# Optimization experiments

Measured on AMD Instinct MI355X. Metric: run time of the kernel, lower is better.

Reference implementation:

```python
import jax, jax.numpy as jnp
import numpy as np

N_NODES = 100000
N_EDGES = 1600000
D = 128
BETA = 0.001
EPS = 1e-12  # F.normalize eps


def setup_inputs() -> dict:
    key = jax.random.key(0)
    k1, k2, k3, k4, k5, k6 = jax.random.split(key, 6)
    stdv = 1.0 / np.sqrt(D)
    return {
        "input": jax.random.normal(k1, (N_NODES, D), dtype=jnp.float32),
        "edge_rows": jax.random.randint(k2, (N_EDGES,), 0, N_NODES, dtype=jnp.int32),
        "edge_cols": jax.random.randint(k3, (N_EDGES,), 0, N_NODES, dtype=jnp.int32),
        "edge_vals": jax.random.uniform(k4, (N_EDGES,), dtype=jnp.float32),
        "weight": jax.random.uniform(k5, (D, D), minval=-stdv, maxval=stdv, dtype=jnp.float32),
        "bias": jax.random.uniform(k6, (D,), minval=-stdv, maxval=stdv, dtype=jnp.float32),
    }


def reference(input, edge_rows, edge_cols, edge_vals, weight, bias):
    # dense projection: [N, D]
    support = input @ weight
    # sparse neighbor aggregation: agg[i] = sum_{(i,j) in E} adj_val * support[j]
    msgs = edge_vals[:, None] * support[edge_cols]          # [E, D]
    agg = jax.ops.segment_sum(msgs, edge_rows, num_segments=input.shape[0])
    # beta-weighted residual blend
    out = BETA * input + (1.0 - BETA) * agg
    # row-wise L2 normalize (torch F.normalize, p=2, dim=1)
    norm = jnp.sqrt(jnp.sum(out * out, axis=1, keepdims=True))
    out = out / jnp.maximum(norm, EPS)
    # bias add
    return out + bias
```

## Files before the change

### kernel.cpp

```cpp
#include <hip/hip_runtime.h>

#define N_NODES 100000
#define N_EDGES 1600000
#define D 128
#define NB 1563
#define NSUB 8
#define SUBCAP 224
#define CAP (NSUB*SUBCAP)
#define NSLICE 8
#define SLICE_W 12500

typedef short bf16x8 __attribute__((ext_vector_type(8)));
typedef float f32x4 __attribute__((ext_vector_type(4)));

__device__ __forceinline__ unsigned short f2bf(float x){
  union { float f; unsigned u; } v; v.f = x;
  unsigned r = v.u + 0x7fffu + ((v.u >> 16) & 1u);
  return (unsigned short)(r >> 16);
}

__device__ __forceinline__ float bf2f(unsigned short h){
  union { unsigned u; float f; } v; v.u = ((unsigned)h) << 16;
  return v.f;
}

__global__ __launch_bounds__(256) void convert_input(const float4* __restrict__ in4,
                                                     ushort4* __restrict__ outb,
                                                     int* __restrict__ cursor,
                                                     const float* __restrict__ W,
                                                     unsigned short* __restrict__ WT){
  int i = blockIdx.x*256 + threadIdx.x;
  if (i < NSUB*NB) cursor[i] = 0;
  if (i < D*D){
    int k = i >> 7, c = i & 127;
    WT[c*128 + k] = f2bf(W[i]);
  }
  float4 a = in4[i];
  ushort4 h;
  h.x = f2bf(a.x); h.y = f2bf(a.y); h.z = f2bf(a.z); h.w = f2bf(a.w);
  outb[i] = h;
}

__global__ __launch_bounds__(256) void scatter_direct(const int* __restrict__ rows,
                                                      const int* __restrict__ cols,
                                                      const float* __restrict__ vals,
                                                      int* __restrict__ cursor,
                                                      int2* __restrict__ edges_s){
  int i = blockIdx.x*256 + threadIdx.x;
  int s = blockIdx.x & (NSUB-1);
  int r = rows[i];
  int b = r >> 6;
  int pos = atomicAdd(&cursor[s*NB + b], 1);
  if (pos < SUBCAP)
    edges_s[(size_t)b*CAP + s*SUBCAP + pos] =
        make_int2(cols[i] | ((r & 63) << 17), __float_as_int(vals[i]));
}

__global__ __launch_bounds__(512) void agg_final(const ushort4* __restrict__ inb4,
                                                 const int* __restrict__ cursor,
                                                 const int2* __restrict__ edges_g,
                                                 const unsigned short* __restrict__ WTg,
                                                 const float* __restrict__ bias,
                                                 float* __restrict__ out){
  __shared__ __align__(16) unsigned char pool[64*136*2];
  __shared__ unsigned short As[64*136];
  __shared__ int rs[NSLICE*64 + 1];
  __shared__ int cur[NSLICE*64];
  __shared__ int wsum[8];
  __shared__ float rsum[2][64];
  int2* st = (int2*)pool;
  unsigned short* Bs = (unsigned short*)pool;

  int t = threadIdx.x;
  int b = blockIdx.x;
  size_t base = (size_t)b * CAP;

  cur[t] = 0;
  __syncthreads();

  int2 held[NSUB];
  int hv = 0;
  #pragma unroll
  for (int s = 0; s < NSUB; ++s){
    int ms = cursor[s*NB + b];
    if (ms > SUBCAP) ms = SUBCAP;
    if (t < ms){
      int2 e = edges_g[base + s*SUBCAP + t];
      held[s] = e;
      hv |= (1 << s);
      int col = e.x & 0x1FFFF;
      int bin = (col / SLICE_W)*64 + (((unsigned)e.x) >> 17);
      atomicAdd(&cur[bin], 1);
    }
  }
  __syncthreads();

  {
    int c = cur[t];
    int w = t >> 6, lane = t & 63;
    int x = c;
    #pragma unroll
    for (int o = 1; o < 64; o <<= 1){
      int y = __shfl_up(x, o);
      if (lane >= o) x += y;
    }
    if (lane == 63) wsum[w] = x;
    __syncthreads();
    int pre = 0;
    #pragma unroll
    for (int ww = 0; ww < 8; ++ww)
      if (ww < w) pre += wsum[ww];
    int excl = pre + x - c;
    rs[t] = excl;
    cur[t] = excl;
    if (t == 511) rs[512] = excl + c;
  }
  __syncthreads();

  #pragma unroll
  for (int s = 0; s < NSUB; ++s){
    if (hv & (1 << s)){
      int2 e = held[s];
      int col = e.x & 0x1FFFF;
      int bin = (col / SLICE_W)*64 + (((unsigned)e.x) >> 17);
      int pos = atomicAdd(&cur[bin], 1);
      st[pos] = e;
    }
  }
  __syncthreads();

  int grp = t >> 5, l = t & 31;
  float4 r0 = make_float4(0.f,0.f,0.f,0.f);
  float4 r1 = make_float4(0.f,0.f,0.f,0.f);
  float4 r2 = make_float4(0.f,0.f,0.f,0.f);
  float4 r3 = make_float4(0.f,0.f,0.f,0.f);

#define EDGE_ACC(E) { \
    int col_ = (E).x & 0x1FFFF; \
    int j_ = (((unsigned)(E).x) >> 17) & 3; \
    float v_ = __int_as_float((E).y); \
    ushort4 X_ = inb4[(size_t)col_*32 + l]; \
    float f0_ = (j_==0)? v_ : 0.f; \
    float f1_ = (j_==1)? v_ : 0.f; \
    float f2_ = (j_==2)? v_ : 0.f; \
    float f3_ = (j_==3)? v_ : 0.f; \
    float xx_ = bf2f(X_.x), xy_ = bf2f(X_.y), xz_ = bf2f(X_.z), xw_ = bf2f(X_.w); \
    r0.x = fmaf(f0_, xx_, r0.x); r0.y = fmaf(f0_, xy_, r0.y); \
    r0.z = fmaf(f0_, xz_, r0.z); r0.w = fmaf(f0_, xw_, r0.w); \
    r1.x = fmaf(f1_, xx_, r1.x); r1.y = fmaf(f1_, xy_, r1.y); \
    r1.z = fmaf(f1_, xz_, r1.z); r1.w = fmaf(f1_, xw_, r1.w); \
    r2.x = fmaf(f2_, xx_, r2.x); r2.y = fmaf(f2_, xy_, r2.y); \
    r2.z = fmaf(f2_, xz_, r2.z); r2.w = fmaf(f2_, xw_, r2.w); \
    r3.x = fmaf(f3_, xx_, r3.x); r3.y = fmaf(f3_, xy_, r3.y); \
    r3.z = fmaf(f3_, xz_, r3.z); r3.w = fmaf(f3_, xw_, r3.w); }

  for (int s = 0; s < NSLICE; ++s){
    int bin0 = (s << 6) + (grp << 2);
    int e = rs[bin0];
    int end = rs[bin0 + 4];
    for (; e + 4 <= end; e += 4){
      int2 E0 = st[e+0], E1 = st[e+1], E2 = st[e+2], E3 = st[e+3];
      EDGE_ACC(E0); EDGE_ACC(E1); EDGE_ACC(E2); EDGE_ACC(E3);
    }
    for (; e < end; ++e){
      int2 E = st[e];
      EDGE_ACC(E);
    }
    __syncthreads();
  }
#undef EDGE_ACC

  {
    ushort4 h;
    h.x = f2bf(r0.x); h.y = f2bf(r0.y); h.z = f2bf(r0.z); h.w = f2bf(r0.w);
    *((ushort4*)&As[(grp*4+0)*136 + l*4]) = h;
    h.x = f2bf(r1.x); h.y = f2bf(r1.y); h.z = f2bf(r1.z); h.w = f2bf(r1.w);
    *((ushort4*)&As[(grp*4+1)*136 + l*4]) = h;
    h.x = f2bf(r2.x); h.y = f2bf(r2.y); h.z = f2bf(r2.z); h.w = f2bf(r2.w);
    *((ushort4*)&As[(grp*4+2)*136 + l*4]) = h;
    h.x = f2bf(r3.x); h.y = f2bf(r3.y); h.z = f2bf(r3.z); h.w = f2bf(r3.w);
    *((ushort4*)&As[(grp*4+3)*136 + l*4]) = h;
  }
  __syncthreads();

  int w = t >> 6, lane = t & 63;
  int wr = w >> 1, wc = w & 1;
  int q = lane >> 4, n = lane & 15;
  int block_row = b * 64;

  #pragma unroll
  for (int i = 0; i < 4; ++i){
    int idx4 = i*512 + t;
    int row = idx4 >> 5, k4 = idx4 & 31;
    int grow = block_row + row;
    ushort4 h = make_ushort4(0,0,0,0);
    if (grow < N_NODES) h = inb4[(size_t)grow*32 + k4];
    *((ushort4*)&Bs[row*136 + k4*4]) = h;
  }

  bf16x8 afr[4];
  #pragma unroll
  for (int ks = 0; ks < 4; ++ks)
    afr[ks] = *((const bf16x8*)&As[(wr*16 + n)*136 + ks*32 + q*8]);

  f32x4 acc[4];
  #pragma unroll
  for (int ct = 0; ct < 4; ++ct) acc[ct] = (f32x4){0.f, 0.f, 0.f, 0.f};
  #pragma unroll
  for (int ct = 0; ct < 4; ++ct){
    #pragma unroll
    for (int ks = 0; ks < 4; ++ks){
      bf16x8 bfr = *((const bf16x8*)(WTg + (wc*64 + ct*16 + n)*128 + ks*32 + q*8));
      acc[ct] = __builtin_amdgcn_mfma_f32_16x16x32_bf16(afr[ks], bfr, acc[ct], 0, 0, 0);
    }
  }
  __syncthreads();

  float v[4][4];
  float s[4] = {0.f, 0.f, 0.f, 0.f};
  #pragma unroll
  for (int reg = 0; reg < 4; ++reg){
    int row_local = wr*16 + q*4 + reg;
    #pragma unroll
    for (int ct = 0; ct < 4; ++ct){
      float inp = bf2f(Bs[row_local*136 + wc*64 + ct*16 + n]);
      float val = fmaf(0.999f, acc[ct][reg], 0.001f * inp);
      v[ct][reg] = val;
      s[reg] = fmaf(val, val, s[reg]);
    }
  }
  #pragma unroll
  for (int reg = 0; reg < 4; ++reg){
    float x = s[reg];
    x += __shfl_xor(x, 1);
    x += __shfl_xor(x, 2);
    x += __shfl_xor(x, 4);
    x += __shfl_xor(x, 8);
    s[reg] = x;
  }
  if (n == 0){
    #pragma unroll
    for (int reg = 0; reg < 4; ++reg)
      rsum[wc][wr*16 + q*4 + reg] = s[reg];
  }
  __syncthreads();

  #pragma unroll
  for (int reg = 0; reg < 4; ++reg){
    int row_local = wr*16 + q*4 + reg;
    int grow = block_row + row_local;
    if (grow >= N_NODES) continue;
    float tot = rsum[0][row_local] + rsum[1][row_local];
    float scale = 1.f / fmaxf(sqrtf(tot), 1e-12f);
    float* outrow = out + (size_t)grow * D;
    #pragma unroll
    for (int ct = 0; ct < 4; ++ct){
      int c = wc*64 + ct*16 + n;
      outrow[c] = fmaf(v[ct][reg], scale, bias[c]);
    }
  }
}

extern "C" void kernel_launch(void* const* d_in, const int* in_sizes, int n_in,
                              void* d_out, int out_size, void* d_ws, size_t ws_size,
                              hipStream_t stream){
  const float* input  = (const float*)d_in[0];
  const int*   erows  = (const int*)d_in[1];
  const int*   ecols  = (const int*)d_in[2];
  const float* evals  = (const float*)d_in[3];
  const float* weight = (const float*)d_in[4];
  const float* bias   = (const float*)d_in[5];
  float* out = (float*)d_out;

  int*   cursor    = (int*)d_ws;
  int2*  edges_s   = (int2*)(cursor + NSUB*NB);
  ushort4* inb     = (ushort4*)(edges_s + (size_t)NB*CAP);
  unsigned short* WTg = (unsigned short*)(inb + (size_t)N_NODES * 32);

  convert_input<<<12500, 256, 0, stream>>>((const float4*)input, inb, cursor, weight, WTg);
  scatter_direct<<<N_EDGES/256, 256, 0, stream>>>(erows, ecols, evals, cursor, edges_s);
  agg_final<<<NB, 512, 0, stream>>>((const ushort4*)inb, cursor, edges_s,
                                    WTg, bias, out);
}
```

Baseline: 308.4 us.

## Assign one 8-thread group per row instead of 32-thread group per four rows

The gather-accumulate phase now gives each destination row its own 8-lane group, with each lane loading four ushort4 chunks of the neighbor row. Before, a 32-lane group handled four rows and applied masked FMAs to all four accumulators for every edge. The change removes the 4x redundant FMA work from masking and stores plain column indices in the sorted edge list. The cost is more independent groups with their own edge-count imbalance, and less coalesced per-lane loads (8 lanes x 4 strided chunks instead of 32 contiguous lanes).

```diff
diff --git a/kernel.cpp b/kernel.cpp
--- a/kernel.cpp
+++ b/kernel.cpp
@@ -124,62 +124,59 @@
       int col = e.x & 0x1FFFF;
       int bin = (col / SLICE_W)*64 + (((unsigned)e.x) >> 17);
       int pos = atomicAdd(&cur[bin], 1);
-      st[pos] = e;
-    }
-  }
-  __syncthreads();
-
-  int grp = t >> 5, l = t & 31;
-  float4 r0 = make_float4(0.f,0.f,0.f,0.f);
-  float4 r1 = make_float4(0.f,0.f,0.f,0.f);
-  float4 r2 = make_float4(0.f,0.f,0.f,0.f);
-  float4 r3 = make_float4(0.f,0.f,0.f,0.f);
-
-#define EDGE_ACC(E) { \
-    int col_ = (E).x & 0x1FFFF; \
-    int j_ = (((unsigned)(E).x) >> 17) & 3; \
-    float v_ = __int_as_float((E).y); \
-    ushort4 X_ = inb4[(size_t)col_*32 + l]; \
-    float f0_ = (j_==0)? v_ : 0.f; \
-    float f1_ = (j_==1)? v_ : 0.f; \
-    float f2_ = (j_==2)? v_ : 0.f; \
-    float f3_ = (j_==3)? v_ : 0.f; \
-    float xx_ = bf2f(X_.x), xy_ = bf2f(X_.y), xz_ = bf2f(X_.z), xw_ = bf2f(X_.w); \
-    r0.x = fmaf(f0_, xx_, r0.x); r0.y = fmaf(f0_, xy_, r0.y); \
-    r0.z = fmaf(f0_, xz_, r0.z); r0.w = fmaf(f0_, xw_, r0.w); \
-    r1.x = fmaf(f1_, xx_, r1.x); r1.y = fmaf(f1_, xy_, r1.y); \
-    r1.z = fmaf(f1_, xz_, r1.z); r1.w = fmaf(f1_, xw_, r1.w); \
-    r2.x = fmaf(f2_, xx_, r2.x); r2.y = fmaf(f2_, xy_, r2.y); \
-    r2.z = fmaf(f2_, xz_, r2.z); r2.w = fmaf(f2_, xw_, r2.w); \
-    r3.x = fmaf(f3_, xx_, r3.x); r3.y = fmaf(f3_, xy_, r3.y); \
-    r3.z = fmaf(f3_, xz_, r3.z); r3.w = fmaf(f3_, xw_, r3.w); }
+      st[pos] = make_int2(col, e.y);
+    }
+  }
+  __syncthreads();
+
+  int g = t >> 3, i8 = t & 7;
+  float4 ac0 = make_float4(0.f,0.f,0.f,0.f);
+  float4 ac1 = make_float4(0.f,0.f,0.f,0.f);
+  float4 ac2 = make_float4(0.f,0.f,0.f,0.f);
+  float4 ac3 = make_float4(0.f,0.f,0.f,0.f);
+
+#define EACC(C, V) { \
+    const ushort4* rp_ = inb4 + (size_t)(C)*32 + i8; \
+    ushort4 Y0_ = rp_[0]; \
+    ushort4 Y1_ = rp_[8]; \
+    ushort4 Y2_ = rp_[16]; \
+    ushort4 Y3_ = rp_[24]; \
+    ac0.x = fmaf((V), bf2f(Y0_.x), ac0.x); ac0.y = fmaf((V), bf2f(Y0_.y), ac0.y); \
+    ac0.z = fmaf((V), bf2f(Y0_.z), ac0.z); ac0.w = fmaf((V), bf2f(Y0_.w), ac0.w); \
+    ac1.x = fmaf((V), bf2f(Y1_.x), ac1.x); ac1.y = fmaf((V), bf2f(Y1_.y), ac1.y); \
+    ac1.z = fmaf((V), bf2f(Y1_.z), ac1.z); ac1.w = fmaf((V), bf2f(Y1_.w), ac1.w); \
+    ac2.x = fmaf((V), bf2f(Y2_.x), ac2.x); ac2.y = fmaf((V), bf2f(Y2_.y), ac2.y); \
+    ac2.z = fmaf((V), bf2f(Y2_.z), ac2.z); ac2.w = fmaf((V), bf2f(Y2_.w), ac2.w); \
+    ac3.x = fmaf((V), bf2f(Y3_.x), ac3.x); ac3.y = fmaf((V), bf2f(Y3_.y), ac3.y); \
+    ac3.z = fmaf((V), bf2f(Y3_.z), ac3.z); ac3.w = fmaf((V), bf2f(Y3_.w), ac3.w); }
 
   for (int s = 0; s < NSLICE; ++s){
-    int bin0 = (s << 6) + (grp << 2);
-    int e = rs[bin0];
-    int end = rs[bin0 + 4];
-    for (; e + 4 <= end; e += 4){
-      int2 E0 = st[e+0], E1 = st[e+1], E2 = st[e+2], E3 = st[e+3];
-      EDGE_ACC(E0); EDGE_ACC(E1); EDGE_ACC(E2); EDGE_ACC(E3);
-    }
-    for (; e < end; ++e){
+    int e = rs[(s << 6) + g];
+    int end = rs[(s << 6) + g + 1];
+    for (; e + 2 <= end; e += 2){
+      int2 E0 = st[e], E1 = st[e+1];
+      float v0 = __int_as_float(E0.y), v1 = __int_as_float(E1.y);
+      EACC(E0.x, v0);
+      EACC(E1.x, v1);
+    }
+    if (e < end){
       int2 E = st[e];
-      EDGE_ACC(E);
+      EACC(E.x, __int_as_float(E.y));
     }
     __syncthreads();
   }
-#undef EDGE_ACC
+#undef EACC
 
   {
     ushort4 h;
-    h.x = f2bf(r0.x); h.y = f2bf(r0.y); h.z = f2bf(r0.z); h.w = f2bf(r0.w);
-    *((ushort4*)&As[(grp*4+0)*136 + l*4]) = h;
-    h.x = f2bf(r1.x); h.y = f2bf(r1.y); h.z = f2bf(r1.z); h.w = f2bf(r1.w);
-    *((ushort4*)&As[(grp*4+1)*136 + l*4]) = h;
-    h.x = f2bf(r2.x); h.y = f2bf(r2.y); h.z = f2bf(r2.z); h.w = f2bf(r2.w);
-    *((ushort4*)&As[(grp*4+2)*136 + l*4]) = h;
-    h.x = f2bf(r3.x); h.y = f2bf(r3.y); h.z = f2bf(r3.z); h.w = f2bf(r3.w);
-    *((ushort4*)&As[(grp*4+3)*136 + l*4]) = h;
+    h.x = f2bf(ac0.x); h.y = f2bf(ac0.y); h.z = f2bf(ac0.z); h.w = f2bf(ac0.w);
+    *((ushort4*)&As[g*136 + (i8   )*4]) = h;
+    h.x = f2bf(ac1.x); h.y = f2bf(ac1.y); h.z = f2bf(ac1.z); h.w = f2bf(ac1.w);
+    *((ushort4*)&As[g*136 + (i8+ 8)*4]) = h;
+    h.x = f2bf(ac2.x); h.y = f2bf(ac2.y); h.z = f2bf(ac2.z); h.w = f2bf(ac2.w);
+    *((ushort4*)&As[g*136 + (i8+16)*4]) = h;
+    h.x = f2bf(ac3.x); h.y = f2bf(ac3.y); h.z = f2bf(ac3.z); h.w = f2bf(ac3.w);
+    *((ushort4*)&As[g*136 + (i8+24)*4]) = h;
   }
   __syncthreads();
 
```

Result: no change. 304.6 us (-1.2%).
